# Kernel optimization log

Measured on AMD Instinct MI355X. Metric: run time of the kernel, lower is better.

Reference implementation:

```python
import jax, jax.numpy as jnp
import numpy as np

B = 16          # number of point clouds
N_COARSE = 1024  # points per cloud at coarse level
N_FINE = 4096    # points per cloud at fine level
C_IN = 256       # coarse feature channels
C_SKIP = 128     # fine skip feature channels
C_HID = 256
EPS = 1e-16


def setup_inputs() -> dict:
    key = jax.random.key(0)
    ks = jax.random.split(key, 8)
    x = jax.random.normal(ks[0], (B * N_COARSE, C_IN), dtype=jnp.float32)
    pos = jax.random.uniform(ks[1], (B * N_COARSE, 3), dtype=jnp.float32)
    x_skip = jax.random.normal(ks[2], (B * N_FINE, C_SKIP), dtype=jnp.float32)
    pos_skip = jax.random.uniform(ks[3], (B * N_FINE, 3), dtype=jnp.float32)
    # uniform batch assignment (sorted), one segment per cloud
    batch = jnp.repeat(jnp.arange(B, dtype=jnp.int32), N_COARSE)
    batch_skip = jnp.repeat(jnp.arange(B, dtype=jnp.int32), N_FINE)
    # MLP params: Linear(384 -> 256) + ReLU, Linear(256 -> 256) + ReLU
    c0 = C_IN + C_SKIP
    W1 = jax.random.normal(ks[4], (c0, C_HID), dtype=jnp.float32) / np.sqrt(c0)
    b1 = jnp.zeros((C_HID,), dtype=jnp.float32)
    W2 = jax.random.normal(ks[5], (C_HID, C_HID), dtype=jnp.float32) / np.sqrt(C_HID)
    b2 = jnp.zeros((C_HID,), dtype=jnp.float32)
    return {"x": x, "pos": pos, "x_skip": x_skip, "pos_skip": pos_skip,
            "W1": W1, "b1": b1, "W2": W2, "b2": b2,
            "batch": batch, "batch_skip": batch_skip, "k": 3}


def _knn_interpolate(x, pos, pos_skip, k):
    # batch is uniform: reshape into [B, n, ...] blocks (same as per-batch kNN)
    xb = x.reshape(B, N_COARSE, -1)          # [B, Nc, C]
    pc = pos.reshape(B, N_COARSE, 3)         # [B, Nc, 3]
    pf = pos_skip.reshape(B, N_FINE, 3)      # [B, Nf, 3]
    # squared pairwise distances within each cloud: [B, Nf, Nc]
    d2 = jnp.sum((pf[:, :, None, :] - pc[:, None, :, :]) ** 2, axis=-1)
    neg_d2, idx = jax.lax.top_k(-d2, k)      # k nearest -> [B, Nf, k]
    w = 1.0 / jnp.maximum(-neg_d2, EPS)      # inverse-squared-distance weights
    gathered = jax.vmap(lambda xc, i: xc[i])(xb, idx)  # [B, Nf, k, C]
    interp = jnp.sum(w[..., None] * gathered, axis=2) / jnp.sum(w, axis=2, keepdims=True)
    return interp.reshape(B * N_FINE, -1)    # [B*Nf, C]


def reference(x, pos, x_skip, pos_skip, W1, b1, W2, b2, batch, batch_skip, k):
    x_up = _knn_interpolate(x, pos, pos_skip, k)
    h = jnp.concatenate([x_up, x_skip], axis=1)          # [B*Nf, C_IN+C_SKIP]
    h = jax.nn.relu(h @ W1 + b1)
    h = jax.nn.relu(h @ W2 + b2)
    return (h, pos_skip, batch_skip)
```

## Files before the change

kernel.cpp:

```cpp
#include <hip/hip_runtime.h>

#define B_ 16
#define NC 1024
#define NF 4096
#define CIN 256
#define CSKIP 128
#define CHID 256
#define MTOT (B_ * NF)
#define EPS_ 1e-16f

typedef _Float16 f16;
typedef __attribute__((ext_vector_type(8))) _Float16 f16x8;
typedef __attribute__((ext_vector_type(4))) _Float16 f16x4;
typedef __attribute__((ext_vector_type(2))) _Float16 f16x2;
typedef __attribute__((ext_vector_type(4))) float f32x4;

__global__ __launch_bounds__(256) void knn_kernel(
    const float* __restrict__ pos, const float* __restrict__ pos_skip,
    int* __restrict__ idx3, float* __restrict__ w3)
{
    __shared__ float4 cpos[NC];
    __shared__ float  cd[64 * 12];
    __shared__ int    ci[64 * 12];

    const int b  = blockIdx.x >> 6;
    const int fb = blockIdx.x & 63;
    const float* cp = pos + (size_t)b * NC * 3;
    for (int i = threadIdx.x; i < NC; i += 256)
        cpos[i] = make_float4(cp[i * 3], cp[i * 3 + 1], cp[i * 3 + 2], 0.0f);
    __syncthreads();

    const int fl = threadIdx.x & 63;
    const int q  = threadIdx.x >> 6;
    const int f  = b * NF + fb * 64 + fl;
    const float px = pos_skip[f * 3 + 0];
    const float py = pos_skip[f * 3 + 1];
    const float pz = pos_skip[f * 3 + 2];

    float d0 = 3.4e38f, d1 = 3.4e38f, d2 = 3.4e38f;
    int   i0 = 0, i1 = 0, i2 = 0;
    const int jbase = q << 8;
#pragma unroll 4
    for (int jj = 0; jj < 256; ++jj) {
        const int j = jbase + jj;
        float4 c = cpos[j];
        float dx = px - c.x, dy = py - c.y, dz = pz - c.z;
        float d = fmaf(dx, dx, fmaf(dy, dy, dz * dz));
        if (d < d2) {
            if (d < d1) {
                d2 = d1; i2 = i1;
                if (d < d0) { d1 = d0; i1 = i0; d0 = d; i0 = j; }
                else        { d1 = d;  i1 = j; }
            } else { d2 = d; i2 = j; }
        }
    }
    const int cb = fl * 12 + q * 3;
    cd[cb + 0] = d0; cd[cb + 1] = d1; cd[cb + 2] = d2;
    ci[cb + 0] = i0; ci[cb + 1] = i1; ci[cb + 2] = i2;
    __syncthreads();

    if (threadIdx.x < 64) {
        float e0 = 3.4e38f, e1 = 3.4e38f, e2 = 3.4e38f;
        int   j0 = 0, j1 = 0, j2 = 0;
#pragma unroll
        for (int s = 0; s < 12; ++s) {
            const float d = cd[fl * 12 + s];
            const int   j = ci[fl * 12 + s];
            if (d < e2) {
                if (d < e1) {
                    e2 = e1; j2 = j1;
                    if (d < e0) { e1 = e0; j1 = j0; e0 = d; j0 = j; }
                    else        { e1 = d;  j1 = j; }
                } else { e2 = d; j2 = j; }
            }
        }
        float w0 = 1.0f / fmaxf(e0, EPS_);
        float w1 = 1.0f / fmaxf(e1, EPS_);
        float w2 = 1.0f / fmaxf(e2, EPS_);
        float inv = 1.0f / (w0 + w1 + w2);
        idx3[f * 3 + 0] = b * NC + j0;
        idx3[f * 3 + 1] = b * NC + j1;
        idx3[f * 3 + 2] = b * NC + j2;
        w3[f * 3 + 0] = w0 * inv;
        w3[f * 3 + 1] = w1 * inv;
        w3[f * 3 + 2] = w2 * inv;
    }
}

__global__ __launch_bounds__(256) void wconv_kernel(
    const float* __restrict__ W1, const float* __restrict__ W2,
    f16* __restrict__ W1aT, f16* __restrict__ W1bT, f16* __restrict__ W2T)
{
    const int t = blockIdx.x * 256 + threadIdx.x;
    if (t < 256 * 256) {
        const int k = t >> 8, n = t & 255;
        W1aT[n * 256 + k] = (f16)W1[k * 256 + n];
    } else if (t < 256 * 256 + 128 * 256) {
        const int u = t - 256 * 256;
        const int k = u >> 8, n = u & 255;
        W1bT[n * 128 + k] = (f16)W1[(256 + k) * 256 + n];
    } else if (t < 256 * 256 + 128 * 256 + 256 * 256) {
        const int u = t - 256 * 256 - 128 * 256;
        const int k = u >> 8, n = u & 255;
        W2T[n * 256 + k] = (f16)W2[k * 256 + n];
    }
}

__device__ __forceinline__ void gload16(const void* g, void* l)
{
    __builtin_amdgcn_global_load_lds(
        (const __attribute__((address_space(1))) unsigned int*)g,
        (__attribute__((address_space(3))) unsigned int*)l, 16, 0, 0);
}

template <int K>
__global__ __launch_bounds__(256, 2) void gemm_regA(
    const float* __restrict__ A, const f16* __restrict__ Bt,
    f16* __restrict__ C)
{
    __shared__ f16 As[128 * 64];
    __shared__ f16 Bs[256 * 64];
    const int tid  = threadIdx.x;
    const int lane = tid & 63;
    const int wid  = tid >> 6;
    const int wr   = wid >> 1, wc = wid & 1;
    const int m0   = blockIdx.x * 128;

    const int srow = tid >> 1;
    const int scg  = tid & 1;
    const int srow_l = lane >> 3;
    const int kch    = (lane & 7) ^ ((lane >> 3) & 7);

    f32x4 acc[4][8] = {};

    for (int k0 = 0; k0 < K; k0 += 64) {
#pragma unroll
        for (int r = 0; r < 8; ++r) {
            const int c = (wid << 3) + r;
            const int row = (c << 3) + srow_l;
            gload16(Bt + (size_t)row * K + k0 + kch * 8,
                    (char*)Bs + (c << 10));
        }
        {
            const float* p = A + (size_t)(m0 + srow) * K + k0 + scg * 32;
            float v[32];
#pragma unroll
            for (int j = 0; j < 8; ++j) {
                float4 a = ((const float4*)p)[j];
                v[j * 4 + 0] = a.x; v[j * 4 + 1] = a.y;
                v[j * 4 + 2] = a.z; v[j * 4 + 3] = a.w;
            }
#pragma unroll
            for (int j = 0; j < 4; ++j) {
                f16x8 hh;
#pragma unroll
                for (int t2 = 0; t2 < 8; ++t2) hh[t2] = (f16)v[j * 8 + t2];
                const int sphys = (scg * 4 + j) ^ (srow & 7);
                *(f16x8*)((char*)As + srow * 128 + sphys * 16) = hh;
            }
        }
        __syncthreads();

#pragma unroll
        for (int h = 0; h < 2; ++h) {
            f16x8 aF[4];
#pragma unroll
            for (int m = 0; m < 4; ++m) {
                const int row  = wr * 64 + m * 16 + (lane & 15);
                const int kg   = (h << 2) + (lane >> 4);
                const int slot = kg ^ (row & 7);
                aF[m] = *(const f16x8*)((const char*)As + row * 128 + slot * 16);
            }
#pragma unroll
            for (int n = 0; n < 8; ++n) {
                const int row  = wc * 128 + n * 16 + (lane & 15);
                const int kg   = (h << 2) + (lane >> 4);
                const int slot = kg ^ (row & 7);
                f16x8 bF = *(const f16x8*)((const char*)Bs + row * 128 + slot * 16);
#pragma unroll
                for (int m = 0; m < 4; ++m)
                    acc[m][n] = __builtin_amdgcn_mfma_f32_16x16x32_f16(
                        aF[m], bF, acc[m][n], 0, 0, 0);
            }
        }
        __syncthreads();
    }

#pragma unroll
    for (int m = 0; m < 4; ++m) {
#pragma unroll
        for (int n = 0; n < 8; ++n) {
            const int col = wc * 128 + n * 16 + (lane & 15);
#pragma unroll
            for (int r = 0; r < 4; ++r) {
                const int row = m0 + wr * 64 + m * 16 + ((lane >> 4) << 2) + r;
                C[(size_t)row * 256 + col] = (f16)acc[m][n][r];
            }
        }
    }
}

__global__ __launch_bounds__(256) void gather_add_relu_kernel(
    const f16* __restrict__ h1pre, const f16* __restrict__ y,
    const int* __restrict__ idx3, const float* __restrict__ w3,
    const float* __restrict__ b1, f16* __restrict__ h1)
{
    const int w = threadIdx.x >> 6, l = threadIdx.x & 63;
    const int m = blockIdx.x * 4 + w;
    const int i0 = idx3[m * 3 + 0], i1 = idx3[m * 3 + 1], i2 = idx3[m * 3 + 2];
    const float w0 = w3[m * 3 + 0], w1 = w3[m * 3 + 1], w2 = w3[m * 3 + 2];
    const int c = l * 4;

    f16x4 hp = *(const f16x4*)&h1pre[(size_t)m * 256 + c];
    f16x4 y0 = *(const f16x4*)&y[(size_t)i0 * 256 + c];
    f16x4 y1 = *(const f16x4*)&y[(size_t)i1 * 256 + c];
    f16x4 y2 = *(const f16x4*)&y[(size_t)i2 * 256 + c];
    float4 bv = *(const float4*)&b1[c];

    f16x4 o;
    o.x = (f16)fmaxf((float)hp.x + w0 * (float)y0.x + w1 * (float)y1.x + w2 * (float)y2.x + bv.x, 0.0f);
    o.y = (f16)fmaxf((float)hp.y + w0 * (float)y0.y + w1 * (float)y1.y + w2 * (float)y2.y + bv.y, 0.0f);
    o.z = (f16)fmaxf((float)hp.z + w0 * (float)y0.z + w1 * (float)y1.z + w2 * (float)y2.z + bv.z, 0.0f);
    o.w = (f16)fmaxf((float)hp.w + w0 * (float)y0.w + w1 * (float)y1.w + w2 * (float)y2.w + bv.w, 0.0f);
    *(f16x4*)&h1[(size_t)m * 256 + c] = o;
}

template <int K>
__global__ __launch_bounds__(256) void gemm_f16_mfma(
    const f16* __restrict__ A, const f16* __restrict__ Bt,
    const float* __restrict__ bias, float* __restrict__ Cout)
{
    __shared__ f16 As[128 * 64];
    __shared__ f16 Bs[128 * 64];
    const int tid  = threadIdx.x;
    const int lane = tid & 63;
    const int wid  = tid >> 6;
    const int wr   = wid >> 1, wc = wid & 1;
    const int m0 = blockIdx.x * 128;
    const int n0 = blockIdx.y * 128;

    const int srow_l = lane >> 3;
    const int kch    = (lane & 7) ^ ((lane >> 3) & 7);

    f32x4 acc[4][4] = {};

    for (int k0 = 0; k0 < K; k0 += 64) {
#pragma unroll
        for (int r = 0; r < 4; ++r) {
            const int c = (wid << 2) + r;
            const int row = (c << 3) + srow_l;
            gload16(A  + (size_t)(m0 + row) * K + k0 + kch * 8,
                    (char*)As + (c << 10));
            gload16(Bt + (size_t)(n0 + row) * K + k0 + kch * 8,
                    (char*)Bs + (c << 10));
        }
        __syncthreads();

#pragma unroll
        for (int h = 0; h < 2; ++h) {
            f16x8 aF[4], bF[4];
#pragma unroll
            for (int m = 0; m < 4; ++m) {
                const int row  = wr * 64 + m * 16 + (lane & 15);
                const int kg   = (h << 2) + (lane >> 4);
                const int slot = kg ^ (row & 7);
                aF[m] = *(const f16x8*)((const char*)As + row * 128 + slot * 16);
            }
#pragma unroll
            for (int n = 0; n < 4; ++n) {
                const int row  = wc * 64 + n * 16 + (lane & 15);
                const int kg   = (h << 2) + (lane >> 4);
                const int slot = kg ^ (row & 7);
                bF[n] = *(const f16x8*)((const char*)Bs + row * 128 + slot * 16);
            }
#pragma unroll
            for (int m = 0; m < 4; ++m)
#pragma unroll
                for (int n = 0; n < 4; ++n)
                    acc[m][n] = __builtin_amdgcn_mfma_f32_16x16x32_f16(
                        aF[m], bF[n], acc[m][n], 0, 0, 0);
        }
        __syncthreads();
    }

#pragma unroll
    for (int m = 0; m < 4; ++m) {
#pragma unroll
        for (int n = 0; n < 4; ++n) {
            const int col = n0 + wc * 64 + n * 16 + (lane & 15);
            const float bv = bias[col];
#pragma unroll
            for (int r = 0; r < 4; ++r) {
                const int row = m0 + wr * 64 + m * 16 + ((lane >> 4) << 2) + r;
                Cout[(size_t)row * 256 + col] = fmaxf(acc[m][n][r] + bv, 0.0f);
            }
        }
    }
}

__global__ __launch_bounds__(256) void copy_tail_kernel(
    const float* __restrict__ pos_skip, const int* __restrict__ batch_skip,
    float* __restrict__ out)
{
    const int i = blockIdx.x * 256 + threadIdx.x;
    const int npos = MTOT * 3;
    if (i < npos)               out[i] = pos_skip[i];
    else if (i < npos + MTOT)   out[i] = (float)batch_skip[i - npos];
}

extern "C" void kernel_launch(void* const* d_in, const int* in_sizes, int n_in,
                              void* d_out, int out_size, void* d_ws, size_t ws_size,
                              hipStream_t stream)
{
    const float* x        = (const float*)d_in[0];
    const float* pos      = (const float*)d_in[1];
    const float* x_skip   = (const float*)d_in[2];
    const float* pos_skip = (const float*)d_in[3];
    const float* W1       = (const float*)d_in[4];
    const float* b1       = (const float*)d_in[5];
    const float* W2       = (const float*)d_in[6];
    const float* b2       = (const float*)d_in[7];
    const int*   batch_skip = (const int*)d_in[9];
    float* out = (float*)d_out;

    char* ws = (char*)d_ws;
    int*   idx3  = (int*)ws;
    float* w3    = (float*)(ws + (1u << 20));
    f16*   W1aT  = (f16*)(ws + (2u << 20));
    f16*   W1bT  = (f16*)(ws + (2u << 20) + (256u << 10));
    f16*   W2T   = (f16*)(ws + (2u << 20) + (512u << 10));
    f16*   y     = (f16*)(ws + (4u << 20));
    f16*   h1pre = (f16*)(ws + (16u << 20));
    f16*   h1    = (f16*)(ws + (48u << 20));

    knn_kernel<<<MTOT / 64, 256, 0, stream>>>(pos, pos_skip, idx3, w3);
    wconv_kernel<<<640, 256, 0, stream>>>(W1, W2, W1aT, W1bT, W2T);

    gemm_regA<256><<<B_ * NC / 128, 256, 0, stream>>>(x, W1aT, y);
    gemm_regA<128><<<MTOT / 128, 256, 0, stream>>>(x_skip, W1bT, h1pre);
    gather_add_relu_kernel<<<MTOT / 4, 256, 0, stream>>>(h1pre, y, idx3, w3, b1, h1);

    dim3 g2(MTOT / 128, 2);
    gemm_f16_mfma<256><<<g2, 256, 0, stream>>>(h1, W2T, b2, out);

    copy_tail_kernel<<<1024, 256, 0, stream>>>(pos_skip, batch_skip,
                                               out + (size_t)MTOT * CHID);
}
```

Baseline: 219.0 us.

## Vectorize layer-1 GEMM stores via permuted hidden layout; full-width layer-2 tiles

The layer-1 GEMM epilogue now writes four f16 values per store instead of scalar stores. The hidden channels end up in a permuted order, and the bias b1 and the K rows of W2 are reordered to match during weight conversion. The layer-2 GEMM is changed to compute all 256 output columns per block (128x256 tile, 2 blocks per CU) instead of two 128-column blocks, so the A tile is read only once. This costs more registers and LDS per block and makes the permutation bookkeeping harder to get right.

```diff
diff --git a/kernel.cpp b/kernel.cpp
--- a/kernel.cpp
+++ b/kernel.cpp
@@ -14,6 +14,7 @@
 typedef __attribute__((ext_vector_type(4))) _Float16 f16x4;
 typedef __attribute__((ext_vector_type(2))) _Float16 f16x2;
 typedef __attribute__((ext_vector_type(4))) float f32x4;
+
 
 __global__ __launch_bounds__(256) void knn_kernel(
     const float* __restrict__ pos, const float* __restrict__ pos_skip,
@@ -89,7 +90,9 @@
 
 __global__ __launch_bounds__(256) void wconv_kernel(
     const float* __restrict__ W1, const float* __restrict__ W2,
-    f16* __restrict__ W1aT, f16* __restrict__ W1bT, f16* __restrict__ W2T)
+    const float* __restrict__ b1,
+    f16* __restrict__ W1aT, f16* __restrict__ W1bT, f16* __restrict__ W2T,
+    float* __restrict__ b1p)
 {
     const int t = blockIdx.x * 256 + threadIdx.x;
     if (t < 256 * 256) {
@@ -101,8 +104,13 @@
         W1bT[n * 128 + k] = (f16)W1[(256 + k) * 256 + n];
     } else if (t < 256 * 256 + 128 * 256 + 256 * 256) {
         const int u = t - 256 * 256 - 128 * 256;
-        const int k = u >> 8, n = u & 255;
-        W2T[n * 256 + k] = (f16)W2[k * 256 + n];
+        const int n = u >> 8, j = u & 255;
+        const int k = (j & ~63) + ((j & 3) << 4) + ((j >> 2) & 15);
+        W2T[n * 256 + j] = (f16)W2[k * 256 + n];
+    } else if (t < 256 * 256 + 128 * 256 + 256 * 256 + 256) {
+        const int j = t - (256 * 256 + 128 * 256 + 256 * 256);
+        const int k = (j & ~63) + ((j & 3) << 4) + ((j >> 2) & 15);
+        b1p[j] = b1[k];
     }
 }
 
@@ -186,15 +194,20 @@
         __syncthreads();
     }
 
+    const int qq = lane & 15;
 #pragma unroll
     for (int m = 0; m < 4; ++m) {
-#pragma unroll
-        for (int n = 0; n < 8; ++n) {
-            const int col = wc * 128 + n * 16 + (lane & 15);
-#pragma unroll
-            for (int r = 0; r < 4; ++r) {
-                const int row = m0 + wr * 64 + m * 16 + ((lane >> 4) << 2) + r;
-                C[(size_t)row * 256 + col] = (f16)acc[m][n][r];
+        const int rb = wr * 64 + m * 16 + ((lane >> 4) << 2);
+#pragma unroll
+        for (int r = 0; r < 4; ++r) {
+            const int rg = m0 + rb + r;
+#pragma unroll
+            for (int g = 0; g < 2; ++g) {
+                f16x4 hv;
+#pragma unroll
+                for (int n = 0; n < 4; ++n)
+                    hv[n] = (f16)acc[m][g * 4 + n][r];
+                *(f16x4*)&C[(size_t)rg * 256 + wc * 128 + g * 64 + qq * 4] = hv;
             }
         }
     }
@@ -203,7 +216,7 @@
 __global__ __launch_bounds__(256) void gather_add_relu_kernel(
     const f16* __restrict__ h1pre, const f16* __restrict__ y,
     const int* __restrict__ idx3, const float* __restrict__ w3,
-    const float* __restrict__ b1, f16* __restrict__ h1)
+    const float* __restrict__ b1p, f16* __restrict__ h1)
 {
     const int w = threadIdx.x >> 6, l = threadIdx.x & 63;
     const int m = blockIdx.x * 4 + w;
@@ -215,7 +228,7 @@
     f16x4 y0 = *(const f16x4*)&y[(size_t)i0 * 256 + c];
     f16x4 y1 = *(const f16x4*)&y[(size_t)i1 * 256 + c];
     f16x4 y2 = *(const f16x4*)&y[(size_t)i2 * 256 + c];
-    float4 bv = *(const float4*)&b1[c];
+    float4 bv = *(const float4*)&b1p[c];
 
     f16x4 o;
     o.x = (f16)fmaxf((float)hp.x + w0 * (float)y0.x + w1 * (float)y1.x + w2 * (float)y2.x + bv.x, 0.0f);
@@ -225,40 +238,43 @@
     *(f16x4*)&h1[(size_t)m * 256 + c] = o;
 }
 
-template <int K>
-__global__ __launch_bounds__(256) void gemm_f16_mfma(
+__global__ __launch_bounds__(256, 2) void gemm2_kernel(
     const f16* __restrict__ A, const f16* __restrict__ Bt,
-    const float* __restrict__ bias, float* __restrict__ Cout)
+    const float* __restrict__ bias, float* __restrict__ out)
 {
     __shared__ f16 As[128 * 64];
-    __shared__ f16 Bs[128 * 64];
+    __shared__ f16 Bs[256 * 64];
     const int tid  = threadIdx.x;
     const int lane = tid & 63;
     const int wid  = tid >> 6;
     const int wr   = wid >> 1, wc = wid & 1;
-    const int m0 = blockIdx.x * 128;
-    const int n0 = blockIdx.y * 128;
+    const int m0   = blockIdx.x * 128;
 
     const int srow_l = lane >> 3;
     const int kch    = (lane & 7) ^ ((lane >> 3) & 7);
 
-    f32x4 acc[4][4] = {};
-
-    for (int k0 = 0; k0 < K; k0 += 64) {
+    f32x4 acc[4][8] = {};
+
+    for (int k0 = 0; k0 < 256; k0 += 64) {
 #pragma unroll
         for (int r = 0; r < 4; ++r) {
             const int c = (wid << 2) + r;
             const int row = (c << 3) + srow_l;
-            gload16(A  + (size_t)(m0 + row) * K + k0 + kch * 8,
+            gload16(A + (size_t)(m0 + row) * 256 + k0 + kch * 8,
                     (char*)As + (c << 10));
-            gload16(Bt + (size_t)(n0 + row) * K + k0 + kch * 8,
+        }
+#pragma unroll
+        for (int r = 0; r < 8; ++r) {
+            const int c = (wid << 3) + r;
+            const int row = (c << 3) + srow_l;
+            gload16(Bt + (size_t)row * 256 + k0 + kch * 8,
                     (char*)Bs + (c << 10));
         }
         __syncthreads();
 
 #pragma unroll
         for (int h = 0; h < 2; ++h) {
-            f16x8 aF[4], bF[4];
+            f16x8 aF[4];
 #pragma unroll
             for (int m = 0; m < 4; ++m) {
                 const int row  = wr * 64 + m * 16 + (lane & 15);
@@ -267,18 +283,16 @@
                 aF[m] = *(const f16x8*)((const char*)As + row * 128 + slot * 16);
             }
 #pragma unroll
-            for (int n = 0; n < 4; ++n) {
-                const int row  = wc * 64 + n * 16 + (lane & 15);
+            for (int n = 0; n < 8; ++n) {
+                const int row  = wc * 128 + n * 16 + (lane & 15);
                 const int kg   = (h << 2) + (lane >> 4);
                 const int slot = kg ^ (row & 7);
-                bF[n] = *(const f16x8*)((const char*)Bs + row * 128 + slot * 16);
-            }
-#pragma unroll
-            for (int m = 0; m < 4; ++m)
-#pragma unroll
-                for (int n = 0; n < 4; ++n)
+                f16x8 bF = *(const f16x8*)((const char*)Bs + row * 128 + slot * 16);
+#pragma unroll
+                for (int m = 0; m < 4; ++m)
                     acc[m][n] = __builtin_amdgcn_mfma_f32_16x16x32_f16(
-                        aF[m], bF[n], acc[m][n], 0, 0, 0);
+                        aF[m], bF, acc[m][n], 0, 0, 0);
+            }
         }
         __syncthreads();
     }
@@ -286,13 +300,13 @@
 #pragma unroll
     for (int m = 0; m < 4; ++m) {
 #pragma unroll
-        for (int n = 0; n < 4; ++n) {
-            const int col = n0 + wc * 64 + n * 16 + (lane & 15);
+        for (int n = 0; n < 8; ++n) {
+            const int col = wc * 128 + n * 16 + (lane & 15);
             const float bv = bias[col];
 #pragma unroll
             for (int r = 0; r < 4; ++r) {
                 const int row = m0 + wr * 64 + m * 16 + ((lane >> 4) << 2) + r;
-                Cout[(size_t)row * 256 + col] = fmaxf(acc[m][n][r] + bv, 0.0f);
+                out[(size_t)row * 256 + col] = fmaxf(acc[m][n][r] + bv, 0.0f);
             }
         }
     }
@@ -329,19 +343,19 @@
     f16*   W1aT  = (f16*)(ws + (2u << 20));
     f16*   W1bT  = (f16*)(ws + (2u << 20) + (256u << 10));
     f16*   W2T   = (f16*)(ws + (2u << 20) + (512u << 10));
+    float* b1p   = (float*)(ws + (2u << 20) + (768u << 10));
     f16*   y     = (f16*)(ws + (4u << 20));
     f16*   h1pre = (f16*)(ws + (16u << 20));
     f16*   h1    = (f16*)(ws + (48u << 20));
 
     knn_kernel<<<MTOT / 64, 256, 0, stream>>>(pos, pos_skip, idx3, w3);
-    wconv_kernel<<<640, 256, 0, stream>>>(W1, W2, W1aT, W1bT, W2T);
+    wconv_kernel<<<641, 256, 0, stream>>>(W1, W2, b1, W1aT, W1bT, W2T, b1p);
 
     gemm_regA<256><<<B_ * NC / 128, 256, 0, stream>>>(x, W1aT, y);
     gemm_regA<128><<<MTOT / 128, 256, 0, stream>>>(x_skip, W1bT, h1pre);
-    gather_add_relu_kernel<<<MTOT / 4, 256, 0, stream>>>(h1pre, y, idx3, w3, b1, h1);
-
-    dim3 g2(MTOT / 128, 2);
-    gemm_f16_mfma<256><<<g2, 256, 0, stream>>>(h1, W2T, b2, out);
+    gather_add_relu_kernel<<<MTOT / 4, 256, 0, stream>>>(h1pre, y, idx3, w3, b1p, h1);
+
+    gemm2_kernel<<<MTOT / 128, 256, 0, stream>>>(h1, W2T, b2, out);
 
     copy_tail_kernel<<<1024, 256, 0, stream>>>(pos_skip, batch_skip,
                                                out + (size_t)MTOT * CHID);
```

New measurement: 216.1 us. No clear change (-1.3%).
